# Kernel optimization log

Measured on AMD Instinct MI355X. Metric: run time of the kernel, lower is better.

The kernel has to match this reference:

```python
import jax, jax.numpy as jnp
import numpy as np

DIM = 1024
DIM_HEAD = 128
HEADS = 8
DIM_INNER = DIM_HEAD * HEADS


def setup_inputs() -> dict:
    key = jax.random.key(0)
    k_x, k_qkv, k_out = jax.random.split(key, 3)
    x = jax.random.normal(k_x, (2, 2048, DIM), dtype=jnp.float32)
    gamma = jnp.ones((DIM,), dtype=jnp.float32)
    # nn.Linear weights stored as [out, in]; init ~ U(-1/sqrt(in), 1/sqrt(in))
    w_qkv = jax.random.uniform(k_qkv, (DIM_INNER * 3, DIM), dtype=jnp.float32,
                               minval=-1.0, maxval=1.0) / np.sqrt(DIM)
    w_out = jax.random.uniform(k_out, (DIM, DIM_INNER), dtype=jnp.float32,
                               minval=-1.0, maxval=1.0) / np.sqrt(DIM_INNER)
    return {"x": x, "gamma": gamma, "w_qkv": w_qkv, "w_out": w_out}


def reference(x, gamma, w_qkv, w_out):
    scale_norm = DIM ** 0.5
    scale_attn = DIM_HEAD ** -0.5
    # RMSNorm as written: F.normalize (L2) * sqrt(dim) * gamma
    l2 = jnp.sqrt(jnp.sum(x * x, axis=-1, keepdims=True))
    xn = x / jnp.maximum(l2, 1e-12) * scale_norm * gamma
    # QKV projection: [b, n, 3*h*d]
    qkv = jnp.einsum('bnc,fc->bnf', xn, w_qkv)
    b, n, _ = qkv.shape
    qkv = qkv.reshape(b, n, 3, HEADS, DIM_HEAD)
    q, k, v = (qkv[:, :, 0], qkv[:, :, 1], qkv[:, :, 2])  # [b, n, h, d]
    q = q * scale_attn
    sim = jnp.einsum('bihd,bjhd->bhij', q, k)
    causal_mask = jnp.triu(jnp.ones((n, n), dtype=bool), k=1)
    neg = -jnp.finfo(sim.dtype).max
    sim = jnp.where(causal_mask, neg, sim)
    attn = jax.nn.softmax(sim, axis=-1)
    out = jnp.einsum('bhij,bjhd->bihd', attn, v)
    out = out.reshape(b, n, DIM_INNER)  # merge heads: b n (h d)
    return jnp.einsum('bnf,cf->bnc', out, w_out)
```

## Files before the change

kernel.cpp:

```cpp
#include <hip/hip_runtime.h>

#define SEQ 2048
#define NTOK 4096
#define DIM 1024
#define FQKV 3072
#define SC_ATTN 0.08838834764831843f
#define SC_Q (0.08838834764831843f * 1.4426950408889634f)
#define SC_NORM 32.0f

typedef short short8 __attribute__((ext_vector_type(8)));
typedef float f32x4 __attribute__((ext_vector_type(4)));
typedef unsigned short u16x4 __attribute__((ext_vector_type(4)));

__device__ __forceinline__ unsigned short f2bf(float f) {
    unsigned int u = __float_as_uint(f);
    u += 0x7fffu + ((u >> 16) & 1u);
    return (unsigned short)(u >> 16);
}
__device__ __forceinline__ void gl_lds16(const void* g, void* l) {
    __builtin_amdgcn_global_load_lds((const __attribute__((address_space(1))) void*)g,
                                     (__attribute__((address_space(3))) void*)l, 16, 0, 0);
}

__global__ __launch_bounds__(256) void l2norm_bf16(const float* __restrict__ x,
                                                   const float* __restrict__ gamma,
                                                   unsigned short* __restrict__ xn) {
    int token = blockIdx.x;
    float4 v = ((const float4*)(x + (size_t)token * DIM))[threadIdx.x];
    float ss = v.x * v.x + v.y * v.y + v.z * v.z + v.w * v.w;
#pragma unroll
    for (int off = 32; off > 0; off >>= 1) ss += __shfl_down(ss, off);
    __shared__ float wsum[4];
    if ((threadIdx.x & 63) == 0) wsum[threadIdx.x >> 6] = ss;
    __syncthreads();
    float tot = wsum[0] + wsum[1] + wsum[2] + wsum[3];
    float sc = SC_NORM / fmaxf(sqrtf(tot), 1e-12f);
    float4 g = ((const float4*)gamma)[threadIdx.x];
    u16x4 o;
    o.x = f2bf(v.x * sc * g.x);
    o.y = f2bf(v.y * sc * g.y);
    o.z = f2bf(v.z * sc * g.z);
    o.w = f2bf(v.w * sc * g.w);
    ((u16x4*)(xn + (size_t)token * DIM))[threadIdx.x] = o;
}

__global__ __launch_bounds__(256) void wconv2(const float* __restrict__ wa, unsigned short* __restrict__ oa, int na4,
                                              const float* __restrict__ wb, unsigned short* __restrict__ ob, int nb4) {
    int i = blockIdx.x * 256 + threadIdx.x;
    const float* w; unsigned short* o; int idx;
    if (i < na4) { w = wa; o = oa; idx = i; }
    else { idx = i - na4; if (idx >= nb4) return; w = wb; o = ob; }
    float4 v = ((const float4*)w)[idx];
    u16x4 r;
    r.x = f2bf(v.x); r.y = f2bf(v.y); r.z = f2bf(v.z); r.w = f2bf(v.w);
    ((u16x4*)o)[idx] = r;
}

template<int C_MODE>
__global__ __launch_bounds__(256) void gemm_bf16(const unsigned short* __restrict__ A,
                                                 const unsigned short* __restrict__ B,
                                                 void* __restrict__ Cv,
                                                 int M, int N, int K) {
    __shared__ unsigned short As[2][128 * 64];
    __shared__ unsigned short Bs[2][128 * 64];
    const int bn = blockIdx.x * 128, bm = blockIdx.y * 128;
    const int tid = threadIdx.x, lane = tid & 63, wv = tid >> 6;
    const int wr = wv >> 1, wc = wv & 1;
    const int l15 = lane & 15, g = lane >> 4;

    f32x4 acc[4][4] = {};

    auto stage = [&](int buf, int k0) {
#pragma unroll
        for (int inst = 0; inst < 4; ++inst) {
            int ci = inst * 256 + wv * 64 + lane;
            int row = ci >> 3, cc = ci & 7;
            int co = (cc ^ (row & 7)) << 3;
            gl_lds16(A + (size_t)(bm + row) * K + k0 + co, &As[buf][(inst * 256 + wv * 64) * 8]);
            gl_lds16(B + (size_t)(bn + row) * K + k0 + co, &Bs[buf][(inst * 256 + wv * 64) * 8]);
        }
    };

    stage(0, 0);
    __syncthreads();
    int cur = 0;
    for (int k0 = 0; k0 < K; k0 += 64) {
        if (k0 + 64 < K) stage(cur ^ 1, k0 + 64);
#pragma unroll
        for (int ks = 0; ks < 2; ++ks) {
            short8 af[4], bf[4];
#pragma unroll
            for (int f = 0; f < 4; ++f) {
                int ra = wr * 64 + f * 16 + l15;
                af[f] = *(const short8*)&As[cur][ra * 64 + (((ks * 4 + g) ^ (ra & 7)) << 3)];
                int rb = wc * 64 + f * 16 + l15;
                bf[f] = *(const short8*)&Bs[cur][rb * 64 + (((ks * 4 + g) ^ (rb & 7)) << 3)];
            }
#pragma unroll
            for (int i = 0; i < 4; ++i)
#pragma unroll
                for (int j = 0; j < 4; ++j)
                    acc[i][j] = __builtin_amdgcn_mfma_f32_16x16x32_bf16(af[i], bf[j], acc[i][j], 0, 0, 0);
        }
        __syncthreads();
        cur ^= 1;
    }

    if (C_MODE == 0) {
        float* C = (float*)Cv;
#pragma unroll
        for (int i = 0; i < 4; ++i)
#pragma unroll
            for (int j = 0; j < 4; ++j)
#pragma unroll
                for (int v = 0; v < 4; ++v) {
                    int row = bm + wr * 64 + i * 16 + g * 4 + v;
                    int col = bn + wc * 64 + j * 16 + l15;
                    C[(size_t)row * N + col] = acc[i][j][v];
                }
    } else {
        unsigned short* C = (unsigned short*)Cv;
        float s = (bn < 1024) ? SC_Q : 1.0f;
#pragma unroll
        for (int i = 0; i < 4; ++i)
#pragma unroll
            for (int j = 0; j < 4; ++j)
#pragma unroll
                for (int v = 0; v < 4; ++v) {
                    int row = bm + wr * 64 + i * 16 + g * 4 + v;
                    int col = bn + wc * 64 + j * 16 + l15;
                    C[(size_t)row * N + col] = f2bf(acc[i][j][v] * s);
                }
    }
}

__global__ __launch_bounds__(256) void transpose_v(const unsigned short* __restrict__ qkv,
                                                   unsigned short* __restrict__ vt) {
    __shared__ unsigned short T[64][72];
    const int t0 = blockIdx.x * 64, d0 = blockIdx.y * 64, bh = blockIdx.z;
    const int b = bh >> 3, h = bh & 7;
    const int tid = threadIdx.x;
#pragma unroll
    for (int p = 0; p < 2; ++p) {
        int r = p * 32 + (tid >> 3), c = tid & 7;
        *(short8*)&T[r][c * 8] =
            *(const short8*)(qkv + (size_t)(b * SEQ + t0 + r) * FQKV + 2048 + h * 128 + d0 + c * 8);
    }
    __syncthreads();
#pragma unroll
    for (int p = 0; p < 2; ++p) {
        int d = p * 32 + (tid >> 3), c = tid & 7;
        short8 v;
#pragma unroll
        for (int j = 0; j < 8; ++j) v[j] = (short)T[c * 8 + j][d];
        *(short8*)(vt + (size_t)(bh * 128 + d0 + d) * SEQ + t0 + c * 8) = v;
    }
}

__global__ __launch_bounds__(256) void attn_mfma(const unsigned short* __restrict__ qkv,
                                                 const unsigned short* __restrict__ vt,
                                                 unsigned short* __restrict__ ao,
                                                 float* __restrict__ po,
                                                 float* __restrict__ pml) {
    __shared__ unsigned short Ks[64 * 128];
    __shared__ unsigned short Vs[128 * 64];
    __shared__ unsigned short Ps[4][16 * 64];
    const int h = blockIdx.y, b = blockIdx.z;
    const int x = blockIdx.x;
    int qblk, jb0, jb1, split, slot;
    if (x < 32) {
        qblk = 31 - (x >> 1);
        int s = x & 1;
        int T = qblk + 1, half = (T + 1) >> 1;
        jb0 = s ? half : 0;
        jb1 = s ? T : half;
        split = 1;
        slot = ((b * 8 + h) * 16 + (qblk - 16)) * 2 + s;
    } else {
        qblk = 47 - x;
        jb0 = 0; jb1 = qblk + 1;
        split = 0; slot = 0;
    }
    const int tid = threadIdx.x, lane = tid & 63, wv = tid >> 6;
    const int l15 = lane & 15, g = lane >> 4;
    const int q0 = qblk * 64;
    const int qrow = q0 + wv * 16 + l15;

    auto stageK = [&](int jb) {
#pragma unroll
        for (int inst = 0; inst < 4; ++inst) {
            int ci = inst * 256 + wv * 64 + lane;
            int rowk = ci >> 4, ck = ci & 15;
            gl_lds16(qkv + (size_t)(b * SEQ + jb * 64 + rowk) * FQKV + 1024 + h * 128
                         + ((ck ^ (rowk & 7)) << 3),
                     &Ks[(inst * 256 + wv * 64) * 8]);
        }
    };
    auto stageV = [&](int jb) {
#pragma unroll
        for (int inst = 0; inst < 4; ++inst) {
            int ci = inst * 256 + wv * 64 + lane;
            int rowv = ci >> 3, cv = ci & 7;
            gl_lds16(vt + (size_t)((b * 8 + h) * 128 + rowv) * SEQ + jb * 64
                        + ((cv ^ (rowv & 7)) << 3),
                     &Vs[(inst * 256 + wv * 64) * 8]);
        }
    };

    short8 qf[4];
    {
        const unsigned short* qb = qkv + (size_t)(b * SEQ + qrow) * FQKV + h * 128;
#pragma unroll
        for (int ks = 0; ks < 4; ++ks) qf[ks] = *(const short8*)(qb + ks * 32 + g * 8);
    }

    float m_r = -1e30f, l_r = 0.f;
    f32x4 o[8] = {};

    stageK(jb0);
    __syncthreads();

    for (int jb = jb0; jb < jb1; ++jb) {
        stageV(jb);

        f32x4 s[4] = {};
        __builtin_amdgcn_s_setprio(1);
#pragma unroll
        for (int ks = 0; ks < 4; ++ks) {
#pragma unroll
            for (int fi = 0; fi < 4; ++fi) {
                int rk = fi * 16 + l15;
                short8 kf = *(const short8*)&Ks[rk * 128 + (((ks * 4 + g) ^ (rk & 7)) << 3)];
                s[fi] = __builtin_amdgcn_mfma_f32_16x16x32_bf16(kf, qf[ks], s[fi], 0, 0, 0);
            }
        }
        __builtin_amdgcn_s_setprio(0);

        if (jb == qblk) {
#pragma unroll
            for (int fi = 0; fi < 4; ++fi)
#pragma unroll
                for (int v = 0; v < 4; ++v) {
                    int kv = q0 + fi * 16 + g * 4 + v;
                    if (kv > qrow) s[fi][v] = -1e30f;
                }
        }

        float mx = -1e30f;
#pragma unroll
        for (int fi = 0; fi < 4; ++fi)
            mx = fmaxf(mx, fmaxf(fmaxf(s[fi][0], s[fi][1]), fmaxf(s[fi][2], s[fi][3])));
        mx = fmaxf(mx, __shfl_xor(mx, 16));
        mx = fmaxf(mx, __shfl_xor(mx, 32));
        if (__any(mx - m_r > 16.0f)) {
            float Mn = fmaxf(m_r, mx);
            float alpha = exp2f(m_r - Mn);
            l_r *= alpha;
            float av[4];
#pragma unroll
            for (int v = 0; v < 4; ++v) av[v] = __shfl(alpha, g * 4 + v);
#pragma unroll
            for (int fn = 0; fn < 8; ++fn) {
                o[fn][0] *= av[0]; o[fn][1] *= av[1]; o[fn][2] *= av[2]; o[fn][3] *= av[3];
            }
            m_r = Mn;
        }

        float ps = 0.f;
#pragma unroll
        for (int fi = 0; fi < 4; ++fi) {
#pragma unroll
            for (int p2 = 0; p2 < 2; ++p2) {
                float e0 = exp2f(s[fi][2 * p2] - m_r);
                float e1 = exp2f(s[fi][2 * p2 + 1] - m_r);
                ps += e0 + e1;
                unsigned short b0 = f2bf(e0), b1 = f2bf(e1);
                int kv = fi * 16 + g * 4 + 2 * p2;
                int addr = l15 * 64 + (((kv >> 3) ^ (l15 & 7)) << 3) + (kv & 7);
                *(unsigned int*)&Ps[wv][addr] = (unsigned int)b0 | ((unsigned int)b1 << 16);
            }
        }
        ps += __shfl_xor(ps, 16);
        ps += __shfl_xor(ps, 32);
        l_r += ps;

        __syncthreads();
        if (jb + 1 < jb1) stageK(jb + 1);

        __builtin_amdgcn_s_setprio(1);
#pragma unroll
        for (int ks = 0; ks < 2; ++ks) {
            short8 pa = *(const short8*)&Ps[wv][l15 * 64 + (((ks * 4 + g) ^ (l15 & 7)) << 3)];
#pragma unroll
            for (int fn = 0; fn < 8; ++fn) {
                int rv = fn * 16 + l15;
                short8 vf = *(const short8*)&Vs[rv * 64 + (((ks * 4 + g) ^ (rv & 7)) << 3)];
                o[fn] = __builtin_amdgcn_mfma_f32_16x16x32_bf16(pa, vf, o[fn], 0, 0, 0);
            }
        }
        __builtin_amdgcn_s_setprio(0);

        __syncthreads();
    }

    if (split) {
        float* od = po + (size_t)slot * (64 * 128);
#pragma unroll
        for (int fn = 0; fn < 8; ++fn)
#pragma unroll
            for (int v = 0; v < 4; ++v)
                od[(wv * 16 + g * 4 + v) * 128 + fn * 16 + l15] = o[fn][v];
        if (g == 0) {
            pml[(size_t)slot * 128 + wv * 16 + l15] = m_r;
            pml[(size_t)slot * 128 + 64 + wv * 16 + l15] = l_r;
        }
    } else {
        float lv[4];
#pragma unroll
        for (int v = 0; v < 4; ++v) lv[v] = 1.0f / __shfl(l_r, g * 4 + v);
#pragma unroll
        for (int fn = 0; fn < 8; ++fn)
#pragma unroll
            for (int v = 0; v < 4; ++v) {
                int row = b * SEQ + q0 + wv * 16 + g * 4 + v;
                ao[(size_t)row * DIM + h * 128 + fn * 16 + l15] = f2bf(o[fn][v] * lv[v]);
            }
    }
}

__global__ __launch_bounds__(256) void attn_combine(const float* __restrict__ po,
                                                    const float* __restrict__ pml,
                                                    unsigned short* __restrict__ ao) {
    int t = blockIdx.x;
    int qi = t & 15, h = (t >> 4) & 7, b = t >> 7;
    int qblk = 16 + qi;
    int slot0 = ((b * 8 + h) * 16 + qi) * 2;
    int row = threadIdx.x >> 2;
    int dp = threadIdx.x & 3;
    float m0 = pml[(size_t)slot0 * 128 + row];
    float l0 = pml[(size_t)slot0 * 128 + 64 + row];
    float m1 = pml[(size_t)(slot0 + 1) * 128 + row];
    float l1 = pml[(size_t)(slot0 + 1) * 128 + 64 + row];
    float M = fmaxf(m0, m1);
    float w0 = exp2f(m0 - M), w1 = exp2f(m1 - M);
    float inv = 1.0f / (w0 * l0 + w1 * l1);
    w0 *= inv; w1 *= inv;
    const float4* O0 = (const float4*)(po + (size_t)slot0 * 8192 + row * 128 + dp * 32);
    const float4* O1 = (const float4*)(po + (size_t)(slot0 + 1) * 8192 + row * 128 + dp * 32);
    unsigned short* dst = ao + ((size_t)(b * SEQ + qblk * 64 + row)) * DIM + h * 128 + dp * 32;
#pragma unroll
    for (int j = 0; j < 8; ++j) {
        float4 a = O0[j], c = O1[j];
        u16x4 r;
        r.x = f2bf(w0 * a.x + w1 * c.x);
        r.y = f2bf(w0 * a.y + w1 * c.y);
        r.z = f2bf(w0 * a.z + w1 * c.z);
        r.w = f2bf(w0 * a.w + w1 * c.w);
        *(u16x4*)(dst + j * 4) = r;
    }
}

extern "C" void kernel_launch(void* const* d_in, const int* in_sizes, int n_in,
                              void* d_out, int out_size, void* d_ws, size_t ws_size,
                              hipStream_t stream) {
    const float* x     = (const float*)d_in[0];
    const float* gamma = (const float*)d_in[1];
    const float* w_qkv = (const float*)d_in[2];
    const float* w_out = (const float*)d_in[3];

    char* ws = (char*)d_ws;
    unsigned short* qkvb = (unsigned short*)ws;
    unsigned short* vtb  = (unsigned short*)(ws + 25165824);
    unsigned short* xnb  = (unsigned short*)(ws + 33554432);
    unsigned short* wqb  = (unsigned short*)(ws + 41943040);
    unsigned short* wob  = (unsigned short*)(ws + 48234496);
    unsigned short* aob  = (unsigned short*)(ws + 50331648);
    float*          pml  = (float*)(ws + 58720256);
    float*          po   = (float*)d_out;

    wconv2<<<4096, 256, 0, stream>>>(w_qkv, wqb, 786432, w_out, wob, 262144);
    l2norm_bf16<<<4096, 256, 0, stream>>>(x, gamma, xnb);
    gemm_bf16<1><<<dim3(24, 32), 256, 0, stream>>>(xnb, wqb, qkvb, NTOK, FQKV, DIM);
    transpose_v<<<dim3(32, 2, 16), 256, 0, stream>>>(qkvb, vtb);
    attn_mfma<<<dim3(48, 8, 2), 256, 0, stream>>>(qkvb, vtb, aob, po, pml);
    attn_combine<<<256, 256, 0, stream>>>(po, pml, aob);
    gemm_bf16<0><<<dim3(8, 32), 256, 0, stream>>>(aob, wob, (float*)d_out, NTOK, DIM, DIM);
}
```

Measured before the change: 123.5 us.

## Single-buffer GEMM LDS with register prefetch, XCD block swizzle, smaller output-projection tile

The GEMM moves from double-buffered LDS to a single buffer. Each k-step's fragments are loaded into registers first, then the next tile is staged while the MFMAs run, with explicit waitcnt and barriers in place of __syncthreads. Block indices are remapped so that consecutive workgroups on an XCD share tiles, which should improve L2 locality. The output projection uses 64-row tiles so 512 blocks replace 256 and fill more CUs. The cost is more registers per thread and hand-placed synchronisation.

```diff
diff --git a/kernel.cpp b/kernel.cpp
--- a/kernel.cpp
+++ b/kernel.cpp
@@ -56,65 +56,83 @@
     ((u16x4*)o)[idx] = r;
 }
 
-template<int C_MODE>
+template<int C_MODE, int TM>
 __global__ __launch_bounds__(256) void gemm_bf16(const unsigned short* __restrict__ A,
                                                  const unsigned short* __restrict__ B,
                                                  void* __restrict__ Cv,
                                                  int M, int N, int K) {
-    __shared__ unsigned short As[2][128 * 64];
-    __shared__ unsigned short Bs[2][128 * 64];
-    const int bn = blockIdx.x * 128, bm = blockIdx.y * 128;
+    constexpr int MF = TM / 32;
+    __shared__ unsigned short As[TM * 64];
+    __shared__ unsigned short Bs[128 * 64];
+
+    int lin = blockIdx.y * gridDim.x + blockIdx.x;
+    int nwg = gridDim.x * gridDim.y;
+    int w = (lin & 7) * (nwg >> 3) + (lin >> 3);
+    int bx = w % gridDim.x, by = w / gridDim.x;
+
+    const int bn = bx * 128, bm = by * TM;
     const int tid = threadIdx.x, lane = tid & 63, wv = tid >> 6;
     const int wr = wv >> 1, wc = wv & 1;
     const int l15 = lane & 15, g = lane >> 4;
 
-    f32x4 acc[4][4] = {};
-
-    auto stage = [&](int buf, int k0) {
-#pragma unroll
-        for (int inst = 0; inst < 4; ++inst) {
-            int ci = inst * 256 + wv * 64 + lane;
+    f32x4 acc[MF][4] = {};
+
+    auto stage = [&](int k0) {
+#pragma unroll
+        for (int ia = 0; ia < TM / 32; ++ia) {
+            int ci = ia * 256 + wv * 64 + lane;
             int row = ci >> 3, cc = ci & 7;
             int co = (cc ^ (row & 7)) << 3;
-            gl_lds16(A + (size_t)(bm + row) * K + k0 + co, &As[buf][(inst * 256 + wv * 64) * 8]);
-            gl_lds16(B + (size_t)(bn + row) * K + k0 + co, &Bs[buf][(inst * 256 + wv * 64) * 8]);
+            gl_lds16(A + (size_t)(bm + row) * K + k0 + co, &As[(ia * 256 + wv * 64) * 8]);
+        }
+#pragma unroll
+        for (int ib = 0; ib < 4; ++ib) {
+            int ci = ib * 256 + wv * 64 + lane;
+            int row = ci >> 3, cc = ci & 7;
+            int co = (cc ^ (row & 7)) << 3;
+            gl_lds16(B + (size_t)(bn + row) * K + k0 + co, &Bs[(ib * 256 + wv * 64) * 8]);
         }
     };
 
-    stage(0, 0);
-    __syncthreads();
-    int cur = 0;
+    stage(0);
+    asm volatile("s_waitcnt vmcnt(0)\ns_barrier" ::: "memory");
+
     for (int k0 = 0; k0 < K; k0 += 64) {
-        if (k0 + 64 < K) stage(cur ^ 1, k0 + 64);
+        short8 af[2][MF], bf[2][4];
 #pragma unroll
         for (int ks = 0; ks < 2; ++ks) {
-            short8 af[4], bf[4];
+#pragma unroll
+            for (int f = 0; f < MF; ++f) {
+                int ra = wr * (TM / 2) + f * 16 + l15;
+                af[ks][f] = *(const short8*)&As[ra * 64 + (((ks * 4 + g) ^ (ra & 7)) << 3)];
+            }
 #pragma unroll
             for (int f = 0; f < 4; ++f) {
-                int ra = wr * 64 + f * 16 + l15;
-                af[f] = *(const short8*)&As[cur][ra * 64 + (((ks * 4 + g) ^ (ra & 7)) << 3)];
                 int rb = wc * 64 + f * 16 + l15;
-                bf[f] = *(const short8*)&Bs[cur][rb * 64 + (((ks * 4 + g) ^ (rb & 7)) << 3)];
-            }
-#pragma unroll
-            for (int i = 0; i < 4; ++i)
+                bf[ks][f] = *(const short8*)&Bs[rb * 64 + (((ks * 4 + g) ^ (rb & 7)) << 3)];
+            }
+        }
+        asm volatile("s_waitcnt lgkmcnt(0)\ns_barrier" ::: "memory");
+        if (k0 + 64 < K) stage(k0 + 64);
+#pragma unroll
+        for (int ks = 0; ks < 2; ++ks)
+#pragma unroll
+            for (int i = 0; i < MF; ++i)
 #pragma unroll
                 for (int j = 0; j < 4; ++j)
-                    acc[i][j] = __builtin_amdgcn_mfma_f32_16x16x32_bf16(af[i], bf[j], acc[i][j], 0, 0, 0);
-        }
-        __syncthreads();
-        cur ^= 1;
+                    acc[i][j] = __builtin_amdgcn_mfma_f32_16x16x32_bf16(af[ks][i], bf[ks][j], acc[i][j], 0, 0, 0);
+        asm volatile("s_waitcnt vmcnt(0)\ns_barrier" ::: "memory");
     }
 
     if (C_MODE == 0) {
         float* C = (float*)Cv;
 #pragma unroll
-        for (int i = 0; i < 4; ++i)
+        for (int i = 0; i < MF; ++i)
 #pragma unroll
             for (int j = 0; j < 4; ++j)
 #pragma unroll
                 for (int v = 0; v < 4; ++v) {
-                    int row = bm + wr * 64 + i * 16 + g * 4 + v;
+                    int row = bm + wr * (TM / 2) + i * 16 + g * 4 + v;
                     int col = bn + wc * 64 + j * 16 + l15;
                     C[(size_t)row * N + col] = acc[i][j][v];
                 }
@@ -122,12 +140,12 @@
         unsigned short* C = (unsigned short*)Cv;
         float s = (bn < 1024) ? SC_Q : 1.0f;
 #pragma unroll
-        for (int i = 0; i < 4; ++i)
+        for (int i = 0; i < MF; ++i)
 #pragma unroll
             for (int j = 0; j < 4; ++j)
 #pragma unroll
                 for (int v = 0; v < 4; ++v) {
-                    int row = bm + wr * 64 + i * 16 + g * 4 + v;
+                    int row = bm + wr * (TM / 2) + i * 16 + g * 4 + v;
                     int col = bn + wc * 64 + j * 16 + l15;
                     C[(size_t)row * N + col] = f2bf(acc[i][j][v] * s);
                 }
@@ -380,9 +398,9 @@
 
     wconv2<<<4096, 256, 0, stream>>>(w_qkv, wqb, 786432, w_out, wob, 262144);
     l2norm_bf16<<<4096, 256, 0, stream>>>(x, gamma, xnb);
-    gemm_bf16<1><<<dim3(24, 32), 256, 0, stream>>>(xnb, wqb, qkvb, NTOK, FQKV, DIM);
+    gemm_bf16<1, 128><<<dim3(24, 32), 256, 0, stream>>>(xnb, wqb, qkvb, NTOK, FQKV, DIM);
     transpose_v<<<dim3(32, 2, 16), 256, 0, stream>>>(qkvb, vtb);
     attn_mfma<<<dim3(48, 8, 2), 256, 0, stream>>>(qkvb, vtb, aob, po, pml);
     attn_combine<<<256, 256, 0, stream>>>(po, pml, aob);
-    gemm_bf16<0><<<dim3(8, 32), 256, 0, stream>>>(aob, wob, (float*)d_out, NTOK, DIM, DIM);
-}
+    gemm_bf16<0, 64><<<dim3(8, 64), 256, 0, stream>>>(aob, wob, (float*)d_out, NTOK, DIM, DIM);
+}
```

New measurement: 119.9 us. 1.03x faster.
